# Kernel tuning notes

Hardware: AMD Instinct MI355X
Metric: run time of the kernel (lower is better)

Reference implementation:

```python
import math
import jax, jax.numpy as jnp
import numpy as np

# ---- module hyperparams (from init_kwargs defaults) ----
NUM_AA, EMB_DIM, K, EXCLUDE = 20, 16, 64, 2
R_ON, R_CUT, DELTA, WALL = 8.0, 10.0, 0.3, 10.0
RHO_MIN, RHO_MAX, RHO_BASE = 1.6, 2.8, 2.0
B, L = 8, 2048
BIG = 1e9  # masks excluded pairs in the distance matrix


def setup_inputs() -> dict:
    key = jax.random.key(0)
    k1, k2, k3 = jax.random.split(key, 3)
    # coordinates scaled to a realistic Angstrom spread so switch/softplus are exercised
    R = jax.random.normal(k1, (B, L, 3), dtype=jnp.float32) * 10.0
    seq = jax.random.randint(k2, (B, L), 0, NUM_AA, dtype=jnp.int64)
    # learned params: AA embedding table + size head (small random weight, bias at rho_base)
    emb_table = jax.random.normal(k3, (NUM_AA, EMB_DIM), dtype=jnp.float32)
    size_w = 0.1 * jax.random.normal(jax.random.fold_in(key, 7), (1, EMB_DIM), dtype=jnp.float32)
    frac = (RHO_BASE - RHO_MIN) / max(1e-6, RHO_MAX - RHO_MIN)
    frac = min(0.999, max(0.001, frac))
    size_b = jnp.full((1,), math.log(frac / (1.0 - frac)), dtype=jnp.float32)
    return {"R": R, "seq": seq, "emb_table": emb_table, "size_w": size_w, "size_b": size_b}


def _rho(s, emb_table, size_w, size_b):
    # per-residue learned radius in [RHO_MIN, RHO_MAX]; s: int indices, any shape
    e = emb_table[s]                                  # (..., EMB_DIM)
    x = jnp.einsum('...d,d->...', e, size_w[0]) + size_b[0]
    return RHO_MIN + (RHO_MAX - RHO_MIN) * jax.nn.sigmoid(x)


def _smooth_switch(r):
    # smoothstep from 1 (r<=R_ON) down to 0 (r>=R_CUT)
    t = jnp.clip((r - R_ON) / (R_CUT - R_ON), 0.0, 1.0)
    return 1.0 - t * t * (3.0 - 2.0 * t)


def reference(R, seq, emb_table, size_w, size_b):
    b, l, _ = R.shape
    # pairwise distances (B, L, L)
    diff = R[:, :, None, :] - R[:, None, :, :]
    D = jnp.sqrt(jnp.maximum(jnp.sum(diff * diff, axis=-1), 1e-12))
    # exclude bonded/near-diagonal pairs |i-j| <= EXCLUDE (includes self)
    idx = jnp.arange(l)
    excl = jnp.abs(idx[:, None] - idx[None, :]) <= EXCLUDE
    Dm = jnp.where(excl[None], BIG, D)
    # K smallest distances per residue -> negate for lax.top_k
    neg_r, j = jax.lax.top_k(-Dm, K)                  # (B, L, K)
    r = -neg_r
    # gather neighbor sequence ids along L
    seq_j = jnp.take_along_axis(jnp.broadcast_to(seq[:, :, None], (b, l, K)), j, axis=1)
    # pair radius r0_ij = rho(s_i) + rho(s_j)
    rho_i = _rho(seq, emb_table, size_w, size_b)[:, :, None]   # (B, L, 1)
    rho_j = _rho(seq_j, emb_table, size_w, size_b)             # (B, L, K)
    r0 = rho_i + rho_j
    rep = WALL * jax.nn.softplus((r0 - r) / (DELTA + 1e-12))
    return (rep * _smooth_switch(r)).sum(axis=(1, 2))          # (B,)
```

## Files before the change

kernel.cpp:

```cpp
#include <hip/hip_runtime.h>
#include <hip/hip_fp16.h>
#include <math.h>

#define LRES 2048
#define NB 8
#define KSEL 64
#define EMBD 16
#define NBIN 128
#define BINSCALE 1.28f
#define BINW 0.78125f
#define NSLOT 16

static __device__ __forceinline__ float fdot2u(unsigned a, unsigned b, float c) {
#if __has_builtin(__builtin_amdgcn_fdot2)
    typedef _Float16 h2f __attribute__((ext_vector_type(2)));
    union { unsigned u; h2f h; } ua, ub;
    ua.u = a; ub.u = b;
    return __builtin_amdgcn_fdot2(ua.h, ub.h, c, false);
#else
    float d;
    asm("v_dot2_f32_f16 %0, %1, %2, %3" : "=v"(d) : "v"(a), "v"(b), "v"(c));
    return d;
#endif
}

static __device__ __forceinline__ unsigned hadd2u(unsigned a, unsigned b) {
    __half2 ha = *(__half2*)&a, hb = *(__half2*)&b;
    __half2 r = __hadd2(ha, hb);
    return *(unsigned*)&r;
}

__global__ void prep_kernel(const float* __restrict__ R,
                            const int* __restrict__ seq,
                            const float* __restrict__ emb,
                            const float* __restrict__ w,
                            const float* __restrict__ bias,
                            uint2* __restrict__ pts) {
    int idx = blockIdx.x * blockDim.x + threadIdx.x;
    if (idx < NB * LRES) {
        int s = seq[idx];
        float x = bias[0];
#pragma unroll
        for (int d = 0; d < EMBD; ++d) x += emb[s * EMBD + d] * w[d];
        float rho = 1.6f + 1.2f / (1.0f + expf(-x));
        __half2 h0 = __floats2half2_rn(R[idx * 3 + 0], R[idx * 3 + 1]);
        __half2 h1 = __floats2half2_rn(R[idx * 3 + 2], rho);
        pts[idx] = make_uint2(*(unsigned*)&h0, *(unsigned*)&h1);
    }
}

#define LDS_FENCE() asm volatile("s_waitcnt lgkmcnt(0)" ::: "memory")

__global__ __launch_bounds__(256, 8) void repel_kernel(const uint2* __restrict__ pts,
                                                       float* __restrict__ partial) {
    const int w    = threadIdx.x >> 6;
    const int lane = threadIdx.x & 63;
    const int row  = blockIdx.x * 4 + w;
    const int b    = row >> 11;
    const int i    = row & (LRES - 1);

    __shared__ unsigned hist[4][NBIN];
    __shared__ unsigned slots[4][NSLOT][64];
    __shared__ unsigned shT[4];
    __shared__ float    shS[4];

    const uint2* __restrict__ P  = pts + (b << 11);
    const uint4* __restrict__ P4 = (const uint4*)P;

    *(uint2*)&hist[w][lane << 1] = make_uint2(0u, 0u);
    if (lane == 0) shT[w] = NBIN - 1;

    const uint2 ci = P[i];
    const unsigned ncxy = ci.x ^ 0x80008000u;
    const unsigned nczv = (ci.y & 0x0000FFFFu) ^ 0x00008000u;
    const float rho_i = __high2float(*(__half2*)&ci.y);

    const int s_i = __builtin_amdgcn_readfirstlane(i);
    const int tlo = ((s_i - 2 > 0) ? (s_i - 2) : 0) >> 7;
    const int thi = ((s_i + 2 < LRES - 1) ? (s_i + 2) : (LRES - 1)) >> 7;

    const unsigned lane2 = (unsigned)lane << 1;
    const unsigned exbits = __float_as_uint(1.0e9f);
    LDS_FENCE();

    unsigned d2u[32];
#pragma unroll
    for (int t = 0; t < 16; ++t) {
        uint4 u = P4[(t << 6) + lane];
        int j0 = (t << 7) + (int)lane2;
        unsigned dxyA = hadd2u(u.x, ncxy);
        unsigned dzA  = hadd2u(u.y, nczv) & 0x0000FFFFu;
        float d2a = fdot2u(dxyA, dxyA, fdot2u(dzA, dzA, 0.0f));
        unsigned dxyB = hadd2u(u.z, ncxy);
        unsigned dzB  = hadd2u(u.w, nczv) & 0x0000FFFFu;
        float d2b = fdot2u(dxyB, dxyB, fdot2u(dzB, dzB, 0.0f));
        unsigned dua = __float_as_uint(d2a);
        unsigned dub = __float_as_uint(d2b);
        if (t == tlo || t == thi) {
            int e0 = j0 - i;     e0 = (e0 < 0) ? -e0 : e0;
            int e1 = j0 + 1 - i; e1 = (e1 < 0) ? -e1 : e1;
            if (e0 <= 2) dua = exbits;
            if (e1 <= 2) dub = exbits;
        }
        d2u[2 * t]     = dua;
        d2u[2 * t + 1] = dub;
        if (dua <= 0x42C7FFFFu)
            atomicAdd(&hist[w][(unsigned)(d2a * BINSCALE)], 1u);
        if (dub <= 0x42C7FFFFu)
            atomicAdd(&hist[w][(unsigned)(d2b * BINSCALE)], 1u);
    }
    LDS_FENCE();

    uint2 hv = *(const uint2*)&hist[w][lane << 1];
    unsigned p = hv.x + hv.y;
    unsigned s = p;
#pragma unroll
    for (int o = 1; o < 64; o <<= 1) {
        unsigned uu = __shfl_up(s, o, 64);
        if (lane >= o) s += uu;
    }
    unsigned e0s = s - p;
    if (s >= KSEL && e0s < KSEL) {
        unsigned sub = (e0s + hv.x >= KSEL) ? 0u : 1u;
        shT[w] = (lane << 1) + sub;
    }
    LDS_FENCE();
    const unsigned T   = shT[w];
    const unsigned tkb = __float_as_uint((float)(T + 1) * BINW);

    unsigned cnt = 0;
#pragma unroll
    for (int m = 0; m < 32; ++m) {
        const unsigned jm  = (unsigned)(((m >> 1) << 7) | (m & 1));
        unsigned val  = (d2u[m] & 0xFFFFF800u) | jm | lane2;
        unsigned sel  = (d2u[m] < tkb) ? 1u : 0u;
        unsigned widx = (cnt > NSLOT - 1) ? (NSLOT - 1) : cnt;
        slots[w][widx][lane] = val;
        cnt += sel;
    }
    LDS_FENCE();

    float acc = 0.0f;
    for (unsigned k = 0; k < cnt; ++k) {
        unsigned key = slots[w][k][lane];
        unsigned j = key & 2047u;
        float d2 = __uint_as_float(key & 0xFFFFF800u);
        float r = __fsqrt_rn(fmaxf(d2, 1e-12f));
        uint2 pj = P[j];
        float rho_j = __high2float(*(__half2*)&pj.y);
        float x = (rho_i + rho_j - r) * (1.0f / 0.3f);
        float sp = fmaxf(x, 0.0f) + __logf(1.0f + __expf(-fabsf(x)));
        float t = fminf(fmaxf((r - 8.0f) * 0.5f, 0.0f), 1.0f);
        float sw = 1.0f - t * t * (3.0f - 2.0f * t);
        acc += 10.0f * sp * sw;
    }
#pragma unroll
    for (int o = 32; o > 0; o >>= 1) acc += __shfl_down(acc, o, 64);

    if (lane == 0) shS[w] = acc;
    __syncthreads();
    if (threadIdx.x == 0)
        partial[blockIdx.x] = shS[0] + shS[1] + shS[2] + shS[3];
}

__global__ void reduce_kernel(const float* __restrict__ partial, float* __restrict__ out) {
    __shared__ float sh[4];
    const int b = blockIdx.x;
    const int tid = threadIdx.x;
    float acc = partial[(b << 9) + tid] + partial[(b << 9) + 256 + tid];
#pragma unroll
    for (int o = 32; o > 0; o >>= 1) acc += __shfl_down(acc, o, 64);
    if ((tid & 63) == 0) sh[tid >> 6] = acc;
    __syncthreads();
    if (tid == 0) out[b] = sh[0] + sh[1] + sh[2] + sh[3];
}

extern "C" void kernel_launch(void* const* d_in, const int* in_sizes, int n_in,
                              void* d_out, int out_size, void* d_ws, size_t ws_size,
                              hipStream_t stream) {
    const float* R    = (const float*)d_in[0];
    const int*   seq  = (const int*)d_in[1];
    const float* emb  = (const float*)d_in[2];
    const float* w    = (const float*)d_in[3];
    const float* bias = (const float*)d_in[4];
    float* out = (float*)d_out;

    uint2* pts     = (uint2*)d_ws;
    float* partial = (float*)((char*)d_ws + NB * LRES * sizeof(uint2));

    prep_kernel<<<(NB * LRES + 255) / 256, 256, 0, stream>>>(R, seq, emb, w, bias, pts);
    repel_kernel<<<NB * LRES / 4, 256, 0, stream>>>(pts, partial);
    reduce_kernel<<<NB, 256, 0, stream>>>(partial, out);
}
```

Before: 88.71 us.

## Fuse prep into repel kernel, stage batch points in LDS, recompute distances

Removes the separate prep kernel. Each 512-thread block now builds a 20-entry rho table and converts the whole batch's 2048 points into fp16 in shared memory, then computes distances from LDS instead of global memory. Slots store 16-bit neighbor indices only, and the final pass recomputes the distance from the LDS point instead of unpacking it from a key. The cost is that every block redundantly converts 2048 points from global memory, and the larger LDS footprint may reduce occupancy.

Result: faster. 84.71 us (-4.5%).

```diff
diff --git a/kernel.cpp b/kernel.cpp
--- a/kernel.cpp
+++ b/kernel.cpp
@@ -6,6 +6,7 @@
 #define NB 8
 #define KSEL 64
 #define EMBD 16
+#define NAA 20
 #define NBIN 128
 #define BINSCALE 1.28f
 #define BINW 0.78125f
@@ -30,47 +31,55 @@
     return *(unsigned*)&r;
 }
 
-__global__ void prep_kernel(const float* __restrict__ R,
-                            const int* __restrict__ seq,
-                            const float* __restrict__ emb,
-                            const float* __restrict__ w,
-                            const float* __restrict__ bias,
-                            uint2* __restrict__ pts) {
-    int idx = blockIdx.x * blockDim.x + threadIdx.x;
-    if (idx < NB * LRES) {
-        int s = seq[idx];
-        float x = bias[0];
-#pragma unroll
-        for (int d = 0; d < EMBD; ++d) x += emb[s * EMBD + d] * w[d];
-        float rho = 1.6f + 1.2f / (1.0f + expf(-x));
-        __half2 h0 = __floats2half2_rn(R[idx * 3 + 0], R[idx * 3 + 1]);
-        __half2 h1 = __floats2half2_rn(R[idx * 3 + 2], rho);
-        pts[idx] = make_uint2(*(unsigned*)&h0, *(unsigned*)&h1);
-    }
-}
-
 #define LDS_FENCE() asm volatile("s_waitcnt lgkmcnt(0)" ::: "memory")
 
-__global__ __launch_bounds__(256, 8) void repel_kernel(const uint2* __restrict__ pts,
-                                                       float* __restrict__ partial) {
-    const int w    = threadIdx.x >> 6;
-    const int lane = threadIdx.x & 63;
-    const int row  = blockIdx.x * 4 + w;
+__global__ __launch_bounds__(512, 8) void repel_kernel(
+    const float* __restrict__ R,
+    const int* __restrict__ seq,
+    const float* __restrict__ emb,
+    const float* __restrict__ wv,
+    const float* __restrict__ bias,
+    float* __restrict__ partial)
+{
+    const int tid  = threadIdx.x;
+    const int w    = tid >> 6;
+    const int lane = tid & 63;
+    const int row  = blockIdx.x * 8 + w;
     const int b    = row >> 11;
     const int i    = row & (LRES - 1);
 
-    __shared__ unsigned hist[4][NBIN];
-    __shared__ unsigned slots[4][NSLOT][64];
-    __shared__ unsigned shT[4];
-    __shared__ float    shS[4];
-
-    const uint2* __restrict__ P  = pts + (b << 11);
-    const uint4* __restrict__ P4 = (const uint4*)P;
-
+    __shared__ uint2          Pl[LRES];
+    __shared__ unsigned       hist[8][NBIN];
+    __shared__ unsigned short slots[8][NSLOT][64];
+    __shared__ float          rho_tab[NAA];
+    __shared__ unsigned       shT[8];
+    __shared__ float          shS[8];
+
+    const float* __restrict__ Rb = R + b * (LRES * 3);
+    const int*   __restrict__ Sb = seq + b * LRES;
+
+    if (tid < NAA) {
+        float x = bias[0];
+#pragma unroll
+        for (int d = 0; d < EMBD; ++d) x += emb[tid * EMBD + d] * wv[d];
+        rho_tab[tid] = 1.6f + 1.2f / (1.0f + __expf(-x));
+    }
     *(uint2*)&hist[w][lane << 1] = make_uint2(0u, 0u);
     if (lane == 0) shT[w] = NBIN - 1;
-
-    const uint2 ci = P[i];
+    __syncthreads();
+
+#pragma unroll
+    for (int k = 0; k < 4; ++k) {
+        int p = (k << 9) + tid;
+        float x = Rb[p * 3 + 0], y = Rb[p * 3 + 1], z = Rb[p * 3 + 2];
+        float rho = rho_tab[Sb[p]];
+        __half2 h0 = __floats2half2_rn(x, y);
+        __half2 h1 = __floats2half2_rn(z, rho);
+        Pl[p] = make_uint2(*(unsigned*)&h0, *(unsigned*)&h1);
+    }
+    __syncthreads();
+
+    const uint2 ci = Pl[i];
     const unsigned ncxy = ci.x ^ 0x80008000u;
     const unsigned nczv = (ci.y & 0x0000FFFFu) ^ 0x00008000u;
     const float rho_i = __high2float(*(__half2*)&ci.y);
@@ -81,8 +90,8 @@
 
     const unsigned lane2 = (unsigned)lane << 1;
     const unsigned exbits = __float_as_uint(1.0e9f);
-    LDS_FENCE();
-
+
+    const uint4* __restrict__ P4 = (const uint4*)Pl;
     unsigned d2u[32];
 #pragma unroll
     for (int t = 0; t < 16; ++t) {
@@ -131,8 +140,8 @@
     unsigned cnt = 0;
 #pragma unroll
     for (int m = 0; m < 32; ++m) {
-        const unsigned jm  = (unsigned)(((m >> 1) << 7) | (m & 1));
-        unsigned val  = (d2u[m] & 0xFFFFF800u) | jm | lane2;
+        const unsigned jm = (unsigned)(((m >> 1) << 7) | (m & 1));
+        unsigned short val = (unsigned short)(jm | lane2);
         unsigned sel  = (d2u[m] < tkb) ? 1u : 0u;
         unsigned widx = (cnt > NSLOT - 1) ? (NSLOT - 1) : cnt;
         slots[w][widx][lane] = val;
@@ -142,11 +151,12 @@
 
     float acc = 0.0f;
     for (unsigned k = 0; k < cnt; ++k) {
-        unsigned key = slots[w][k][lane];
-        unsigned j = key & 2047u;
-        float d2 = __uint_as_float(key & 0xFFFFF800u);
-        float r = __fsqrt_rn(fmaxf(d2, 1e-12f));
-        uint2 pj = P[j];
+        unsigned j = slots[w][k][lane];
+        uint2 pj = Pl[j];
+        unsigned dxy = hadd2u(pj.x, ncxy);
+        unsigned dz  = hadd2u(pj.y, nczv) & 0x0000FFFFu;
+        float d2 = fdot2u(dxy, dxy, fdot2u(dz, dz, 0.0f));
+        float r  = __fsqrt_rn(fmaxf(d2, 1e-12f));
         float rho_j = __high2float(*(__half2*)&pj.y);
         float x = (rho_i + rho_j - r) * (1.0f / 0.3f);
         float sp = fmaxf(x, 0.0f) + __logf(1.0f + __expf(-fabsf(x)));
@@ -159,15 +169,19 @@
 
     if (lane == 0) shS[w] = acc;
     __syncthreads();
-    if (threadIdx.x == 0)
-        partial[blockIdx.x] = shS[0] + shS[1] + shS[2] + shS[3];
+    if (tid == 0) {
+        float v = 0.0f;
+#pragma unroll
+        for (int q = 0; q < 8; ++q) v += shS[q];
+        partial[blockIdx.x] = v;
+    }
 }
 
 __global__ void reduce_kernel(const float* __restrict__ partial, float* __restrict__ out) {
     __shared__ float sh[4];
     const int b = blockIdx.x;
     const int tid = threadIdx.x;
-    float acc = partial[(b << 9) + tid] + partial[(b << 9) + 256 + tid];
+    float acc = partial[(b << 8) + tid];
 #pragma unroll
     for (int o = 32; o > 0; o >>= 1) acc += __shfl_down(acc, o, 64);
     if ((tid & 63) == 0) sh[tid >> 6] = acc;
@@ -185,10 +199,8 @@
     const float* bias = (const float*)d_in[4];
     float* out = (float*)d_out;
 
-    uint2* pts     = (uint2*)d_ws;
-    float* partial = (float*)((char*)d_ws + NB * LRES * sizeof(uint2));
-
-    prep_kernel<<<(NB * LRES + 255) / 256, 256, 0, stream>>>(R, seq, emb, w, bias, pts);
-    repel_kernel<<<NB * LRES / 4, 256, 0, stream>>>(pts, partial);
+    float* partial = (float*)d_ws;
+
+    repel_kernel<<<NB * LRES / 8, 512, 0, stream>>>(R, seq, emb, w, bias, partial);
     reduce_kernel<<<NB, 256, 0, stream>>>(partial, out);
 }
```
